# Kernel optimization log

Measured on AMD Instinct MI355X. Metric: run time of the kernel, lower is better.

Reference implementation:

```python
import jax, jax.numpy as jnp
import numpy as np

N, D, O, H, T, S, R, BN = 4096, 256, 256, 256, 512, 8, 4, 2  # nodes, in, out, hidden, text_len, adj_size, relations used, basis_num


def setup_inputs() -> dict:
    key = jax.random.key(0)
    ks = jax.random.split(key, 16)
    sc = 0.05
    return {
        "entity_embeddings": jax.random.normal(ks[0], (N, D), jnp.float32) * sc,
        "text_encodings": jax.random.normal(ks[1], (1, T, 2 * H), jnp.float32) * sc,
        "adj_to_use": jnp.arange(R, dtype=jnp.int32),
        "adj_masks": jax.random.randint(ks[2], (R, N, N), 0, 2, dtype=jnp.int32),
        "text_guids": jax.random.normal(ks[3], (S, 2 * H), jnp.float32) * sc,
        "graph_guids_1": jax.random.normal(ks[4], (S, D), jnp.float32) * sc,
        "graph_guids_2": jax.random.normal(ks[5], (S, D), jnp.float32) * sc,
        "guid_a": jax.random.normal(ks[6], (S,), jnp.float32),
        "basis_V": jax.random.normal(ks[7], (D, BN, O), jnp.float32) * sc,
        "basis_b": jax.random.normal(ks[8], (S, BN), jnp.float32) * sc,
        "W_1": jax.random.normal(ks[9], (2 * H, D), jnp.float32) * sc,
        "W_2": jax.random.normal(ks[10], (2 * H, D), jnp.float32) * sc,
        "ln_gamma": jnp.ones((O,), jnp.float32),
        "ln_beta": jnp.zeros((O,), jnp.float32),
    }


def reference(entity_embeddings, text_encodings, adj_to_use, adj_masks,
              text_guids, graph_guids_1, graph_guids_2, guid_a,
              basis_V, basis_b, W_1, W_2, ln_gamma, ln_beta):
    te = text_encodings[0]                                  # [T, 2H] (batch of 1)
    tg = text_guids[adj_to_use]                             # [R, 2H]
    # text attention: softmax over T, per relation
    att = jax.nn.softmax(te @ tg.T, axis=0)                 # [T, R]
    context = att.T @ te                                    # [R, 2H]
    c1 = context @ W_1                                      # [R, D]
    c2 = context @ W_2
    ga = jax.nn.sigmoid(guid_a[adj_to_use])[:, None]        # [R, 1]
    g1 = ga * graph_guids_1[adj_to_use] + (1.0 - ga) * c1   # [R, D]
    g2 = ga * graph_guids_2[adj_to_use] + (1.0 - ga) * c2
    s1 = entity_embeddings @ g1.T                           # [N, R]
    s2 = entity_embeddings @ g2.T
    # A[r,i,j] = s1[i,r] + s2[j,r], masked softmax over j
    A = s1.T[:, :, None] + s2.T[:, None, :]                 # [R, N, N]
    A = jnp.where(adj_masks == 1, A, jnp.float32(-1e10))
    A = jax.nn.softmax(A, axis=-1)
    fused = jnp.einsum('rij,jd->rid', A, entity_embeddings) # [R, N, D]
    # torch.cat over relations on last dim -> column index r*D + d
    fused_cat = jnp.transpose(fused, (1, 0, 2)).reshape(N, R * D)
    # torch.matmul([R,BN],[D,BN,O]) -> [D,R,O], then .view(R*D, O) (row index d*R + r)
    bb = basis_b[adj_to_use]                                # [R, BN]
    W = jnp.einsum('rb,dbo->dro', bb, basis_V).reshape(D * R, O)
    out = fused_cat @ W                                     # [N, O]
    mu = jnp.mean(out, axis=-1, keepdims=True)
    var = jnp.var(out, axis=-1, keepdims=True)
    out = (out - mu) / jnp.sqrt(var + 1e-5) * ln_gamma + ln_beta
    return jax.nn.relu(out)
```

## Files before the change

### kernel.cpp

```cpp
#include <hip/hip_runtime.h>
#include <hip/hip_bf16.h>


typedef unsigned short u16;
typedef short bf16x8 __attribute__((ext_vector_type(8)));
typedef float f32x4 __attribute__((ext_vector_type(4)));
typedef int   v4i   __attribute__((ext_vector_type(4)));
typedef unsigned int v2u __attribute__((ext_vector_type(2)));

#define G2_OFF    0
#define E2_OFF    4096
#define WRT_OFF   69632
#define FPT_OFF   593920
#define FUSED_OFF 9506816
#define CAN_OFF   26284032
#define ATT_OFF   29443584
#define CTX_OFF   29451776

#define C_ENT 0
#define C_TE  1048576
#define C_TG  1310720
#define C_GG2 1314816
#define C_GA  1316864
#define C_BV  1316872
#define C_BB  1447944
#define C_W2  1447960
#define C_GAM 1579032
#define C_BET 1579288

__device__ __forceinline__ float b2f(u16 u) {
    union { unsigned int i; float f; } v; v.i = ((unsigned int)u) << 16; return v.f;
}
__device__ __forceinline__ u16 f2b(float f) {
    union { float f; unsigned int i; } v; v.f = f;
    return (u16)((v.i + 0x7FFFu + ((v.i >> 16) & 1u)) >> 16);
}
__device__ __forceinline__ void bsync() {
    __builtin_amdgcn_s_waitcnt(0xC07F);
    __builtin_amdgcn_s_barrier();
}

__global__ __launch_bounds__(256) void k_cvt(
    const void* s0, const void* s1, const void* s2, const void* s3,
    const void* s4, const void* s5, const void* s6, const void* s7,
    const void* s8, const void* s9, const unsigned* __restrict__ graw,
    u16* __restrict__ dst)
{
    bool isbf = (graw[0] == 0x3F803F80u);
    const void* srcs[10] = {s0, s1, s2, s3, s4, s5, s6, s7, s8, s9};
    const int ns[10]     = {1048576, 262144, 4096, 2048, 8, 131072, 16, 131072, 256, 256};
    const int offs[10]   = {C_ENT, C_TE, C_TG, C_GG2, C_GA, C_BV, C_BB, C_W2, C_GAM, C_BET};
    const int bstart[11] = {0, 512, 640, 642, 643, 644, 708, 709, 773, 774, 775};
    int b = blockIdx.x, a = 0;
    while (b >= bstart[a + 1]) ++a;
    int rel = b - bstart[a];
    int n = ns[a];
    u16* d = dst + offs[a];
    int base = rel * 2048 + threadIdx.x;
    if (isbf) {
        const u16* s = (const u16*)srcs[a];
        for (int k = 0; k < 8; ++k) { int i = base + k * 256; if (i < n) d[i] = s[i]; }
    } else {
        const float* s = (const float*)srcs[a];
        for (int k = 0; k < 8; ++k) { int i = base + k * 256; if (i < n) d[i] = f2b(s[i]); }
    }
}

__global__ __launch_bounds__(512) void k_pre(const u16* __restrict__ te,
                                             const int* __restrict__ adj,
                                             const u16* __restrict__ tguids,
                                             float* __restrict__ att_ws) {
    __shared__ float s_tg[4 * 512];
    __shared__ float s_att[512 * 4];
    __shared__ float s_red[512 * 4];
    int tid = threadIdx.x;
    int a[4] = {adj[0], adj[1], adj[2], adj[3]};
    for (int k = 0; k < 4; ++k) {
        int idx = tid + k * 512; int r = idx >> 9, h = idx & 511;
        s_tg[r * 512 + h] = b2f(tguids[a[r] * 512 + h]);
    }
    __syncthreads();
    {
        float s[4] = {0.f, 0.f, 0.f, 0.f};
        const u16* row = te + tid * 512;
        for (int h8 = 0; h8 < 512; h8 += 8) {
            v4i pk = *(const v4i*)(row + h8);
            const u16* pu = (const u16*)&pk;
            #pragma unroll
            for (int j = 0; j < 8; ++j) {
                float tv = b2f(pu[j]);
                s[0] += tv * s_tg[h8 + j];        s[1] += tv * s_tg[512 + h8 + j];
                s[2] += tv * s_tg[1024 + h8 + j]; s[3] += tv * s_tg[1536 + h8 + j];
            }
        }
        for (int r = 0; r < 4; ++r) { s_att[tid * 4 + r] = s[r]; s_red[tid * 4 + r] = s[r]; }
    }
    __syncthreads();
    for (int st = 256; st > 0; st >>= 1) {
        if (tid < st) for (int r = 0; r < 4; ++r)
            s_red[tid * 4 + r] = fmaxf(s_red[tid * 4 + r], s_red[(tid + st) * 4 + r]);
        __syncthreads();
    }
    float mx[4]; for (int r = 0; r < 4; ++r) mx[r] = s_red[r];
    __syncthreads();
    for (int r = 0; r < 4; ++r) {
        float e = __expf(s_att[tid * 4 + r] - mx[r]);
        s_att[tid * 4 + r] = e; s_red[tid * 4 + r] = e;
    }
    __syncthreads();
    for (int st = 256; st > 0; st >>= 1) {
        if (tid < st) for (int r = 0; r < 4; ++r)
            s_red[tid * 4 + r] += s_red[(tid + st) * 4 + r];
        __syncthreads();
    }
    float dn[4]; for (int r = 0; r < 4; ++r) dn[r] = s_red[r];
    for (int r = 0; r < 4; ++r) att_ws[tid * 4 + r] = s_att[tid * 4 + r] / dn[r];
}

__global__ __launch_bounds__(256) void k_ctx(const u16* __restrict__ te,
                                             const float* __restrict__ att,
                                             float* __restrict__ ctx) {
    __shared__ float s_att[2048];
    int tid = threadIdx.x, b = blockIdx.x;
    for (int k = 0; k < 8; ++k) s_att[tid + k * 256] = att[tid + k * 256];
    __syncthreads();
    int r = tid >> 6, h = b * 64 + (tid & 63);
    float acc = 0.f;
    #pragma unroll 4
    for (int t = 0; t < 512; ++t) acc += s_att[t * 4 + r] * b2f(te[t * 512 + h]);
    ctx[r * 512 + h] = acc;
}

__global__ __launch_bounds__(256) void k_g2(const float* __restrict__ ctx,
                                            const int* __restrict__ adj,
                                            const u16* __restrict__ gg2,
                                            const u16* __restrict__ guida,
                                            const u16* __restrict__ W2,
                                            float* __restrict__ g2ws) {
    __shared__ float s_c[512];
    int r = blockIdx.x, d = threadIdx.x;
    s_c[d] = ctx[r * 512 + d]; s_c[d + 256] = ctx[r * 512 + 256 + d];
    __syncthreads();
    float acc = 0.f;
    #pragma unroll 4
    for (int h = 0; h < 512; ++h) acc += s_c[h] * b2f(W2[h * 256 + d]);
    int a = adj[r];
    float gav = 1.f / (1.f + expf(-b2f(guida[a])));
    g2ws[r * 256 + d] = gav * b2f(gg2[a * 256 + d]) + (1.f - gav) * acc;
}

__global__ __launch_bounds__(256) void k_s2_wrt(const u16* __restrict__ entity,
                                                const int* __restrict__ adj,
                                                const u16* __restrict__ basisV,
                                                const u16* __restrict__ basisb,
                                                const float* __restrict__ g2ws,
                                                float* __restrict__ e2ws,
                                                u16* __restrict__ wrt) {
    int b = blockIdx.x, tid = threadIdx.x;
    if (b < 64) {
        int j = b * 64 + (tid >> 2), r = tid & 3;
        const u16* erow = entity + j * 256;
        const float* g2r = g2ws + r * 256;
        float acc = 0.f;
        for (int d = 0; d < 256; ++d) acc += b2f(erow[d]) * g2r[d];
        e2ws[r * 4096 + j] = expf(acc);
    } else {
        int b2 = b - 64; int r = b2 >> 6;
        int c = (b2 & 63) * 4 + (tid >> 6);
        int dq = tid & 63;
        int dbase = dq * 4;
        int a[4] = {adj[0], adj[1], adj[2], adj[3]};
        for (int dd = 0; dd < 4; ++dd) {
            float w = 0.f;
            for (int bi = 0; bi < 2; ++bi)
                w += b2f(basisb[a[dd] * 2 + bi]) * b2f(basisV[((64 * r + dq) * 2 + bi) * 256 + c]);
            wrt[(r * 256 + c) * 256 + dbase + dd] = f2b(w);
        }
    }
}

__global__ __launch_bounds__(256) void k_fplus(const u16* __restrict__ entity,
                                               const u16* __restrict__ wrt,
                                               const float* __restrict__ e2ws,
                                               u16* __restrict__ fpt) {
    int b = blockIdx.x, tid = threadIdx.x;
    if (b < 256) {
        int r = b & 3, ct = (b >> 2) & 3, jt = b >> 4;
        int c0 = ct * 64, j0 = jt * 256;
        __shared__ __align__(16) u16 lw[64 * 264];
        const u16* wr = wrt + (r * 256 + c0) * 256;
        for (int k = 0; k < 8; ++k) {
            int ci = tid + k * 256; int row = ci >> 5, off = (ci & 31) * 8;
            *(v4i*)(&lw[row * 264 + off]) = *(const v4i*)(wr + row * 256 + off);
        }
        __syncthreads();
        int wave = tid >> 6, ln = tid & 15, q = (tid & 63) >> 4;
        f32x4 acc[4][4] = {};
        for (int ks = 0; ks < 8; ++ks) {
            bf16x8 afr[4], bfr[4];
            for (int mt = 0; mt < 4; ++mt)
                afr[mt] = *(const bf16x8*)(&lw[(mt * 16 + ln) * 264 + ks * 32 + q * 8]);
            for (int nt = 0; nt < 4; ++nt) {
                int j = j0 + (wave * 4 + nt) * 16 + ln;
                bfr[nt] = *(const bf16x8*)(entity + j * 256 + ks * 32 + q * 8);
            }
            for (int mt = 0; mt < 4; ++mt)
                for (int nt = 0; nt < 4; ++nt)
                    acc[mt][nt] = __builtin_amdgcn_mfma_f32_16x16x32_bf16(afr[mt], bfr[nt], acc[mt][nt], 0, 0, 0);
        }
        for (int nt = 0; nt < 4; ++nt) {
            int j = j0 + (wave * 4 + nt) * 16 + ln;
            float e2j = e2ws[r * 4096 + j];
            int kt = j >> 5, kk = j & 31;
            u16* dst = fpt + (((size_t)(r * 128 + kt)) * 272 << 5);
            for (int mt = 0; mt < 4; ++mt)
                for (int reg = 0; reg < 4; ++reg) {
                    int c = c0 + mt * 16 + q * 4 + reg;
                    dst[(c << 5) + kk] = f2b(acc[mt][nt][reg] * e2j);
                }
        }
    } else {
        int b2 = b - 256; int r = b2 >> 1, half = b2 & 1;
        const float* e2r = e2ws + r * 4096;
        for (int it = 0; it < 128; ++it) {
            int l = it * 256 + tid;
            int kk = l & 31;
            int c  = 256 + ((l >> 5) & 15);
            int kt = half * 64 + (l >> 9);
            fpt[(((size_t)(r * 128 + kt) * 272 + c) << 5) + kk] =
                (c == 256) ? f2b(e2r[kt * 32 + kk]) : (u16)0;
        }
    }
}

__global__ __launch_bounds__(512) void k_big(const int* __restrict__ masks,
                                             const u16* __restrict__ fpt,
                                             float* __restrict__ fused) {
    __shared__ __align__(16) u16 lm2[2][64 * 32];
    __shared__ __align__(16) u16 lf2[2][272 * 32];
    __shared__ float lden[64];
    int b = blockIdx.x, tid = threadIdx.x;
    int xcd = b & 7; int r = xcd & 3;
    int it = (b >> 3) + ((xcd >> 2) << 5);
    long i0 = (long)it * 64;
    const int* mbase = masks + ((long)r << 24) + i0 * 4096;
    const u16* fbase = fpt + (size_t)r * 128 * 272 * 32;
    int mrow = tid >> 3, mch = tid & 7;
    int wave = tid >> 6, lane = tid & 63, ln = lane & 15, q = lane >> 4;
    int mg = wave >> 2, ng = wave & 3;

    f32x4 acc[2][4] = {};
    f32x4 accD0 = {}, accD1 = {};

    v4i pmA, p0A, p1A, p2A, pmB, p0B, p1B, p2B;
    auto load_set = [&](int kt, v4i& pm_, v4i& p0, v4i& p1, v4i& p2) {
        pm_ = __builtin_nontemporal_load((const v4i*)(mbase + mrow * 4096 + kt * 32 + mch * 4));
        const u16* su = fbase + (size_t)kt * 8704;
        p0 = *(const v4i*)(su + tid * 8);
        p1 = *(const v4i*)(su + 4096 + tid * 8);
        if (tid < 64) p2 = *(const v4i*)(su + 8192 + tid * 8);
    };
    auto write_set = [&](int buf, const v4i& pm_, const v4i& p0, const v4i& p1, const v4i& p2) {
        unsigned m0 = (unsigned)pm_.x * 0x3F80u, m1 = (unsigned)pm_.y * 0x3F80u;
        unsigned m2 = (unsigned)pm_.z * 0x3F80u, m3 = (unsigned)pm_.w * 0x3F80u;
        v2u w; w.x = m0 | (m1 << 16); w.y = m2 | (m3 << 16);
        *(v2u*)(&lm2[buf][mrow * 32 + mch * 4]) = w;
        *(v4i*)(&lf2[buf][tid * 8]) = p0;
        *(v4i*)(&lf2[buf][4096 + tid * 8]) = p1;
        if (tid < 64) *(v4i*)(&lf2[buf][8192 + tid * 8]) = p2;
    };
    auto mfma_step = [&](int buf) {
        const u16* lm = lm2[buf];
        const u16* lf = lf2[buf];
        bf16x8 a0 = *(const bf16x8*)(lm + (mg * 32 + ln) * 32 + q * 8);
        bf16x8 a1 = *(const bf16x8*)(lm + (mg * 32 + 16 + ln) * 32 + q * 8);
        #pragma unroll
        for (int nt = 0; nt < 4; ++nt) {
            bf16x8 bf = *(const bf16x8*)(lf + ((ng * 4 + nt) * 16 + ln) * 32 + q * 8);
            acc[0][nt] = __builtin_amdgcn_mfma_f32_16x16x32_bf16(a0, bf, acc[0][nt], 0, 0, 0);
            acc[1][nt] = __builtin_amdgcn_mfma_f32_16x16x32_bf16(a1, bf, acc[1][nt], 0, 0, 0);
        }
        if (ng == 3) {
            bf16x8 bf = *(const bf16x8*)(lf + (256 + ln) * 32 + q * 8);
            accD0 = __builtin_amdgcn_mfma_f32_16x16x32_bf16(a0, bf, accD0, 0, 0, 0);
            accD1 = __builtin_amdgcn_mfma_f32_16x16x32_bf16(a1, bf, accD1, 0, 0, 0);
        }
    };

    load_set(0, pmA, p0A, p1A, p2A);
    load_set(1, pmB, p0B, p1B, p2B);
    write_set(0, pmA, p0A, p1A, p2A);
    load_set(2, pmA, p0A, p1A, p2A);
    bsync();

    #pragma unroll 1
    for (int kt = 0; kt < 128; kt += 2) {
        write_set(1, pmB, p0B, p1B, p2B);
        if (kt + 3 < 128) load_set(kt + 3, pmB, p0B, p1B, p2B);
        mfma_step(0);
        bsync();
        if (kt + 2 < 128) write_set(0, pmA, p0A, p1A, p2A);
        if (kt + 4 < 128) load_set(kt + 4, pmA, p0A, p1A, p2A);
        mfma_step(1);
        bsync();
    }

    if (ng == 3 && ln == 0) {
        #pragma unroll
        for (int reg = 0; reg < 4; ++reg) {
            lden[mg * 32 + q * 4 + reg]      = accD0[reg];
            lden[mg * 32 + 16 + q * 4 + reg] = accD1[reg];
        }
    }
    bsync();
    float* fb = fused + ((long)r * 4096 + i0) * 256;
    #pragma unroll
    for (int mt = 0; mt < 2; ++mt) {
        float rd[4];
        #pragma unroll
        for (int reg = 0; reg < 4; ++reg) rd[reg] = 1.0f / lden[mg * 32 + mt * 16 + q * 4 + reg];
        #pragma unroll
        for (int nt = 0; nt < 4; ++nt) {
            int c = (ng * 4 + nt) * 16 + ln;
            #pragma unroll
            for (int reg = 0; reg < 4; ++reg) {
                int row = mg * 32 + mt * 16 + q * 4 + reg;
                __builtin_nontemporal_store(acc[mt][nt][reg] * rd[reg], fb + row * 256 + c);
            }
        }
    }
}

__global__ __launch_bounds__(256) void k_ln(const float* __restrict__ fused,
                                            const u16* __restrict__ gamma,
                                            const u16* __restrict__ beta,
                                            const unsigned* __restrict__ graw,
                                            void* __restrict__ outraw) {
    __shared__ float wsum[4], wsum2[4];
    int i = blockIdx.x, o = threadIdx.x, w = o >> 6, l = o & 63;
    float x = 0.f;
    for (int r = 0; r < 4; ++r)
        x += __builtin_nontemporal_load(fused + ((long)(r << 12) + i) * 256 + o);
    float s = x, s2 = x * x;
    #pragma unroll
    for (int d = 1; d < 64; d <<= 1) { s += __shfl_xor(s, d); s2 += __shfl_xor(s2, d); }
    if (l == 0) { wsum[w] = s; wsum2[w] = s2; }
    __syncthreads();
    float tot  = wsum[0] + wsum[1] + wsum[2] + wsum[3];
    float tot2 = wsum2[0] + wsum2[1] + wsum2[2] + wsum2[3];
    float mu = tot * (1.f / 256.f);
    float var = tot2 * (1.f / 256.f) - mu * mu;
    float y = (x - mu) * rsqrtf(var + 1e-5f) * b2f(gamma[o]) + b2f(beta[o]);
    float res = fmaxf(y, 0.f);
    bool isbf = (graw[0] == 0x3F803F80u);
    if (isbf) ((u16*)outraw)[i * 256 + o] = f2b(res);
    else      ((float*)outraw)[i * 256 + o] = res;
}

extern "C" void kernel_launch(void* const* d_in, const int* in_sizes, int n_in,
                              void* d_out, int out_size, void* d_ws, size_t ws_size,
                              hipStream_t stream) {
    const int* adj   = (const int*)d_in[2];
    const int* masks = (const int*)d_in[3];
    const unsigned* graw = (const unsigned*)d_in[12];
    char* ws = (char*)d_ws;
    float* g2ws = (float*)(ws + G2_OFF);
    float* e2ws = (float*)(ws + E2_OFF);
    u16*   wrt  = (u16*)(ws + WRT_OFF);
    u16*   fpt  = (u16*)(ws + FPT_OFF);
    float* fus  = (float*)(ws + FUSED_OFF);
    u16*   can  = (u16*)(ws + CAN_OFF);
    float* attw = (float*)(ws + ATT_OFF);
    float* ctxw = (float*)(ws + CTX_OFF);

    k_cvt<<<775, 256, 0, stream>>>(d_in[0], d_in[1], d_in[4], d_in[6], d_in[7],
                                   d_in[8], d_in[9], d_in[11], d_in[12], d_in[13],
                                   graw, can);
    const u16* entity = can + C_ENT;
    const u16* te     = can + C_TE;
    const u16* tguids = can + C_TG;
    const u16* gg2    = can + C_GG2;
    const u16* guida  = can + C_GA;
    const u16* basisV = can + C_BV;
    const u16* basisb = can + C_BB;
    const u16* W2     = can + C_W2;
    const u16* gamma  = can + C_GAM;
    const u16* beta   = can + C_BET;

    k_pre<<<1, 512, 0, stream>>>(te, adj, tguids, attw);
    k_ctx<<<8, 256, 0, stream>>>(te, attw, ctxw);
    k_g2<<<4, 256, 0, stream>>>(ctxw, adj, gg2, guida, W2, g2ws);
    k_s2_wrt<<<320, 256, 0, stream>>>(entity, adj, basisV, basisb, g2ws, e2ws, wrt);
    k_fplus<<<264, 256, 0, stream>>>(entity, wrt, e2ws, fpt);
    k_big<<<256, 512, 0, stream>>>(masks, fpt, fus);
    k_ln<<<4096, 256, 0, stream>>>(fus, gamma, beta, graw, d_out);
}
```

Baseline: 560.5 us.

## Split k_big K-loop in two halves and read B operand directly from global

The main masked-softmax-aggregation kernel now splits the 4096-long reduction into two halves across twice as many blocks (512 instead of 256). Each half writes unnormalized numerators and denominators to workspace, and the layernorm kernel combines them and divides. The B-operand tile is no longer staged through LDS; waves load it straight from global or L2 into registers, which shrinks shared memory so more blocks fit per CU. This trades doubled partial-output traffic and unbuffered global B loads for more parallelism on the 256-CU device.

```diff
diff --git a/kernel.cpp b/kernel.cpp
--- a/kernel.cpp
+++ b/kernel.cpp
@@ -12,10 +12,11 @@
 #define E2_OFF    4096
 #define WRT_OFF   69632
 #define FPT_OFF   593920
-#define FUSED_OFF 9506816
-#define CAN_OFF   26284032
-#define ATT_OFF   29443584
-#define CTX_OFF   29451776
+#define NUM_OFF   9506816
+#define DEN_OFF   43061248
+#define CAN_OFF   43192320
+#define ATT_OFF   46351424
+#define CTX_OFF   46359616
 
 #define C_ENT 0
 #define C_TE  1048576
@@ -233,18 +234,20 @@
     }
 }
 
-__global__ __launch_bounds__(512) void k_big(const int* __restrict__ masks,
-                                             const u16* __restrict__ fpt,
-                                             float* __restrict__ fused) {
+__global__ __launch_bounds__(512, 4) void k_big(const int* __restrict__ masks,
+                                                const u16* __restrict__ fpt,
+                                                float* __restrict__ num,
+                                                float* __restrict__ den) {
     __shared__ __align__(16) u16 lm2[2][64 * 32];
-    __shared__ __align__(16) u16 lf2[2][272 * 32];
-    __shared__ float lden[64];
     int b = blockIdx.x, tid = threadIdx.x;
     int xcd = b & 7; int r = xcd & 3;
-    int it = (b >> 3) + ((xcd >> 2) << 5);
+    int z = b >> 3;
+    int half = z & 1;
+    int it = (z >> 1) + ((xcd >> 2) << 5);
     long i0 = (long)it * 64;
-    const int* mbase = masks + ((long)r << 24) + i0 * 4096;
-    const u16* fbase = fpt + (size_t)r * 128 * 272 * 32;
+    int k0 = half * 64;
+    const int* mbase = masks + ((long)r << 24) + i0 * 4096 + k0 * 32;
+    const u16* fbase = fpt + (size_t)r * 128 * 8704 + (size_t)k0 * 8704;
     int mrow = tid >> 3, mch = tid & 7;
     int wave = tid >> 6, lane = tid & 63, ln = lane & 15, q = lane >> 4;
     int mg = wave >> 2, ng = wave & 3;
@@ -252,86 +255,79 @@
     f32x4 acc[2][4] = {};
     f32x4 accD0 = {}, accD1 = {};
 
-    v4i pmA, p0A, p1A, p2A, pmB, p0B, p1B, p2B;
-    auto load_set = [&](int kt, v4i& pm_, v4i& p0, v4i& p1, v4i& p2) {
-        pm_ = __builtin_nontemporal_load((const v4i*)(mbase + mrow * 4096 + kt * 32 + mch * 4));
-        const u16* su = fbase + (size_t)kt * 8704;
-        p0 = *(const v4i*)(su + tid * 8);
-        p1 = *(const v4i*)(su + 4096 + tid * 8);
-        if (tid < 64) p2 = *(const v4i*)(su + 8192 + tid * 8);
+    v4i sA, sB;
+    auto loadS = [&](int kt, v4i& s) {
+        s = __builtin_nontemporal_load((const v4i*)(mbase + mrow * 4096 + kt * 32 + mch * 4));
     };
-    auto write_set = [&](int buf, const v4i& pm_, const v4i& p0, const v4i& p1, const v4i& p2) {
-        unsigned m0 = (unsigned)pm_.x * 0x3F80u, m1 = (unsigned)pm_.y * 0x3F80u;
-        unsigned m2 = (unsigned)pm_.z * 0x3F80u, m3 = (unsigned)pm_.w * 0x3F80u;
+    auto writeLM = [&](int buf, const v4i& s) {
+        unsigned m0 = (unsigned)s.x * 0x3F80u, m1 = (unsigned)s.y * 0x3F80u;
+        unsigned m2 = (unsigned)s.z * 0x3F80u, m3 = (unsigned)s.w * 0x3F80u;
         v2u w; w.x = m0 | (m1 << 16); w.y = m2 | (m3 << 16);
         *(v2u*)(&lm2[buf][mrow * 32 + mch * 4]) = w;
-        *(v4i*)(&lf2[buf][tid * 8]) = p0;
-        *(v4i*)(&lf2[buf][4096 + tid * 8]) = p1;
-        if (tid < 64) *(v4i*)(&lf2[buf][8192 + tid * 8]) = p2;
     };
-    auto mfma_step = [&](int buf) {
-        const u16* lm = lm2[buf];
-        const u16* lf = lf2[buf];
-        bf16x8 a0 = *(const bf16x8*)(lm + (mg * 32 + ln) * 32 + q * 8);
-        bf16x8 a1 = *(const bf16x8*)(lm + (mg * 32 + 16 + ln) * 32 + q * 8);
-        #pragma unroll
-        for (int nt = 0; nt < 4; ++nt) {
-            bf16x8 bf = *(const bf16x8*)(lf + ((ng * 4 + nt) * 16 + ln) * 32 + q * 8);
-            acc[0][nt] = __builtin_amdgcn_mfma_f32_16x16x32_bf16(a0, bf, acc[0][nt], 0, 0, 0);
-            acc[1][nt] = __builtin_amdgcn_mfma_f32_16x16x32_bf16(a1, bf, acc[1][nt], 0, 0, 0);
-        }
+    auto compute = [&](int buf, int kt) {
+        const u16* su = fbase + (size_t)kt * 8704;
+        bf16x8 b0 = *(const bf16x8*)(su + ((ng * 4 + 0) * 16 + ln) * 32 + q * 8);
+        bf16x8 b1 = *(const bf16x8*)(su + ((ng * 4 + 1) * 16 + ln) * 32 + q * 8);
+        bf16x8 b2 = *(const bf16x8*)(su + ((ng * 4 + 2) * 16 + ln) * 32 + q * 8);
+        bf16x8 b3 = *(const bf16x8*)(su + ((ng * 4 + 3) * 16 + ln) * 32 + q * 8);
+        bf16x8 a0 = *(const bf16x8*)(&lm2[buf][(mg * 32 + ln) * 32 + q * 8]);
+        bf16x8 a1 = *(const bf16x8*)(&lm2[buf][(mg * 32 + 16 + ln) * 32 + q * 8]);
+        acc[0][0] = __builtin_amdgcn_mfma_f32_16x16x32_bf16(a0, b0, acc[0][0], 0, 0, 0);
+        acc[1][0] = __builtin_amdgcn_mfma_f32_16x16x32_bf16(a1, b0, acc[1][0], 0, 0, 0);
+        acc[0][1] = __builtin_amdgcn_mfma_f32_16x16x32_bf16(a0, b1, acc[0][1], 0, 0, 0);
+        acc[1][1] = __builtin_amdgcn_mfma_f32_16x16x32_bf16(a1, b1, acc[1][1], 0, 0, 0);
+        acc[0][2] = __builtin_amdgcn_mfma_f32_16x16x32_bf16(a0, b2, acc[0][2], 0, 0, 0);
+        acc[1][2] = __builtin_amdgcn_mfma_f32_16x16x32_bf16(a1, b2, acc[1][2], 0, 0, 0);
+        acc[0][3] = __builtin_amdgcn_mfma_f32_16x16x32_bf16(a0, b3, acc[0][3], 0, 0, 0);
+        acc[1][3] = __builtin_amdgcn_mfma_f32_16x16x32_bf16(a1, b3, acc[1][3], 0, 0, 0);
         if (ng == 3) {
-            bf16x8 bf = *(const bf16x8*)(lf + (256 + ln) * 32 + q * 8);
-            accD0 = __builtin_amdgcn_mfma_f32_16x16x32_bf16(a0, bf, accD0, 0, 0, 0);
-            accD1 = __builtin_amdgcn_mfma_f32_16x16x32_bf16(a1, bf, accD1, 0, 0, 0);
+            bf16x8 bd = *(const bf16x8*)(su + (256 + ln) * 32 + q * 8);
+            accD0 = __builtin_amdgcn_mfma_f32_16x16x32_bf16(a0, bd, accD0, 0, 0, 0);
+            accD1 = __builtin_amdgcn_mfma_f32_16x16x32_bf16(a1, bd, accD1, 0, 0, 0);
         }
     };
 
-    load_set(0, pmA, p0A, p1A, p2A);
-    load_set(1, pmB, p0B, p1B, p2B);
-    write_set(0, pmA, p0A, p1A, p2A);
-    load_set(2, pmA, p0A, p1A, p2A);
+    loadS(0, sA); loadS(1, sB);
+    writeLM(0, sA);
+    loadS(2, sA);
     bsync();
-
     #pragma unroll 1
-    for (int kt = 0; kt < 128; kt += 2) {
-        write_set(1, pmB, p0B, p1B, p2B);
-        if (kt + 3 < 128) load_set(kt + 3, pmB, p0B, p1B, p2B);
-        mfma_step(0);
+    for (int kt = 0; kt < 64; kt += 2) {
+        writeLM(1, sB);
+        if (kt + 3 < 64) loadS(kt + 3, sB);
+        compute(0, kt);
         bsync();
-        if (kt + 2 < 128) write_set(0, pmA, p0A, p1A, p2A);
-        if (kt + 4 < 128) load_set(kt + 4, pmA, p0A, p1A, p2A);
-        mfma_step(1);
+        if (kt + 2 < 64) writeLM(0, sA);
+        if (kt + 4 < 64) loadS(kt + 4, sA);
+        compute(1, kt + 1);
         bsync();
     }
 
-    if (ng == 3 && ln == 0) {
-        #pragma unroll
-        for (int reg = 0; reg < 4; ++reg) {
-            lden[mg * 32 + q * 4 + reg]      = accD0[reg];
-            lden[mg * 32 + 16 + q * 4 + reg] = accD1[reg];
-        }
-    }
-    bsync();
-    float* fb = fused + ((long)r * 4096 + i0) * 256;
+    float* nb = num + (((size_t)(half * 4 + r) * 4096) + i0) * 256;
     #pragma unroll
-    for (int mt = 0; mt < 2; ++mt) {
-        float rd[4];
-        #pragma unroll
-        for (int reg = 0; reg < 4; ++reg) rd[reg] = 1.0f / lden[mg * 32 + mt * 16 + q * 4 + reg];
+    for (int mt = 0; mt < 2; ++mt)
         #pragma unroll
         for (int nt = 0; nt < 4; ++nt) {
             int c = (ng * 4 + nt) * 16 + ln;
             #pragma unroll
             for (int reg = 0; reg < 4; ++reg) {
                 int row = mg * 32 + mt * 16 + q * 4 + reg;
-                __builtin_nontemporal_store(acc[mt][nt][reg] * rd[reg], fb + row * 256 + c);
+                __builtin_nontemporal_store(acc[mt][nt][reg], nb + row * 256 + c);
             }
         }
-    }
-}
-
-__global__ __launch_bounds__(256) void k_ln(const float* __restrict__ fused,
+    if (ng == 3 && ln == 0) {
+        float* db = den + ((size_t)(half * 4 + r) * 4096) + i0;
+        #pragma unroll
+        for (int reg = 0; reg < 4; ++reg) {
+            db[mg * 32 + q * 4 + reg]      = accD0[reg];
+            db[mg * 32 + 16 + q * 4 + reg] = accD1[reg];
+        }
+    }
+}
+
+__global__ __launch_bounds__(256) void k_ln(const float* __restrict__ num,
+                                            const float* __restrict__ den,
                                             const u16* __restrict__ gamma,
                                             const u16* __restrict__ beta,
                                             const unsigned* __restrict__ graw,
@@ -339,8 +335,13 @@
     __shared__ float wsum[4], wsum2[4];
     int i = blockIdx.x, o = threadIdx.x, w = o >> 6, l = o & 63;
     float x = 0.f;
-    for (int r = 0; r < 4; ++r)
-        x += __builtin_nontemporal_load(fused + ((long)(r << 12) + i) * 256 + o);
+    #pragma unroll
+    for (int r = 0; r < 4; ++r) {
+        float dsum = den[(size_t)r * 4096 + i] + den[(size_t)(4 + r) * 4096 + i];
+        float n = __builtin_nontemporal_load(num + ((size_t)r * 4096 + i) * 256 + o)
+                + __builtin_nontemporal_load(num + ((size_t)(4 + r) * 4096 + i) * 256 + o);
+        x += n / dsum;
+    }
     float s = x, s2 = x * x;
     #pragma unroll
     for (int d = 1; d < 64; d <<= 1) { s += __shfl_xor(s, d); s2 += __shfl_xor(s2, d); }
@@ -368,7 +369,8 @@
     float* e2ws = (float*)(ws + E2_OFF);
     u16*   wrt  = (u16*)(ws + WRT_OFF);
     u16*   fpt  = (u16*)(ws + FPT_OFF);
-    float* fus  = (float*)(ws + FUSED_OFF);
+    float* numw = (float*)(ws + NUM_OFF);
+    float* denw = (float*)(ws + DEN_OFF);
     u16*   can  = (u16*)(ws + CAN_OFF);
     float* attw = (float*)(ws + ATT_OFF);
     float* ctxw = (float*)(ws + CTX_OFF);
@@ -392,6 +394,6 @@
     k_g2<<<4, 256, 0, stream>>>(ctxw, adj, gg2, guida, W2, g2ws);
     k_s2_wrt<<<320, 256, 0, stream>>>(entity, adj, basisV, basisb, g2ws, e2ws, wrt);
     k_fplus<<<264, 256, 0, stream>>>(entity, wrt, e2ws, fpt);
-    k_big<<<256, 512, 0, stream>>>(masks, fpt, fus);
-    k_ln<<<4096, 256, 0, stream>>>(fus, gamma, beta, graw, d_out);
-}
+    k_big<<<512, 512, 0, stream>>>(masks, fpt, numw, denw);
+    k_ln<<<4096, 256, 0, stream>>>(numw, denw, gamma, beta, graw, d_out);
+}
```

After: 586.8 us. 4.7% more time.

## Drop LDS staging in k_big; load MFMA operands directly from global

Applied to the files above, without the earlier changes.

The main masked-aggregation kernel no longer stages the mask and feature tiles through double-buffered shared memory with barriers. Each wave now loads its own mask rows and B fragments straight from global memory into registers, prefetching one k-step ahead, and converts the int mask to bf16 in registers. Blocks shrink to 256 threads covering 32 rows, with twice as many blocks, removing per-step barriers and LDS traffic. In exchange, the feature tile is re-read from global or L2 by every block and wave without sharing, which risks more memory traffic. Smaller tweaks vectorize the e2 dot-product loads and unroll the LayerNorm relation loop.

```diff
diff --git a/kernel.cpp b/kernel.cpp
--- a/kernel.cpp
+++ b/kernel.cpp
@@ -6,7 +6,6 @@
 typedef short bf16x8 __attribute__((ext_vector_type(8)));
 typedef float f32x4 __attribute__((ext_vector_type(4)));
 typedef int   v4i   __attribute__((ext_vector_type(4)));
-typedef unsigned int v2u __attribute__((ext_vector_type(2)));
 
 #define G2_OFF    0
 #define E2_OFF    4096
@@ -35,9 +34,13 @@
     union { float f; unsigned int i; } v; v.f = f;
     return (u16)((v.i + 0x7FFFu + ((v.i >> 16) & 1u)) >> 16);
 }
-__device__ __forceinline__ void bsync() {
-    __builtin_amdgcn_s_waitcnt(0xC07F);
-    __builtin_amdgcn_s_barrier();
+__device__ __forceinline__ bf16x8 cvt8(v4i lo, v4i hi) {
+    v4i p;
+    p.x = (lo.x | (lo.y << 16)) * 0x3F80;
+    p.y = (lo.z | (lo.w << 16)) * 0x3F80;
+    p.z = (hi.x | (hi.y << 16)) * 0x3F80;
+    p.w = (hi.z | (hi.w << 16)) * 0x3F80;
+    union { v4i i; bf16x8 h; } u; u.i = p; return u.h;
 }
 
 __global__ __launch_bounds__(256) void k_cvt(
@@ -162,7 +165,12 @@
         const u16* erow = entity + j * 256;
         const float* g2r = g2ws + r * 256;
         float acc = 0.f;
-        for (int d = 0; d < 256; ++d) acc += b2f(erow[d]) * g2r[d];
+        for (int d8 = 0; d8 < 256; d8 += 8) {
+            v4i pk = *(const v4i*)(erow + d8);
+            const u16* pu = (const u16*)&pk;
+            #pragma unroll
+            for (int jj = 0; jj < 8; ++jj) acc += b2f(pu[jj]) * g2r[d8 + jj];
+        }
         e2ws[r * 4096 + j] = expf(acc);
     } else {
         int b2 = b - 64; int r = b2 >> 6;
@@ -233,98 +241,89 @@
     }
 }
 
-__global__ __launch_bounds__(512) void k_big(const int* __restrict__ masks,
-                                             const u16* __restrict__ fpt,
-                                             float* __restrict__ fused) {
-    __shared__ __align__(16) u16 lm2[2][64 * 32];
-    __shared__ __align__(16) u16 lf2[2][272 * 32];
-    __shared__ float lden[64];
+__global__ __launch_bounds__(256, 3) void k_big(const int* __restrict__ masks,
+                                                const u16* __restrict__ fpt,
+                                                float* __restrict__ fused) {
+    __shared__ float lden[32];
     int b = blockIdx.x, tid = threadIdx.x;
     int xcd = b & 7; int r = xcd & 3;
-    int it = (b >> 3) + ((xcd >> 2) << 5);
-    long i0 = (long)it * 64;
+    int it = (b >> 3) + ((xcd >> 2) << 6);
+    long i0 = (long)it * 32;
     const int* mbase = masks + ((long)r << 24) + i0 * 4096;
-    const u16* fbase = fpt + (size_t)r * 128 * 272 * 32;
-    int mrow = tid >> 3, mch = tid & 7;
+    const u16* fbase = fpt + (size_t)r * 128 * 8704;
     int wave = tid >> 6, lane = tid & 63, ln = lane & 15, q = lane >> 4;
-    int mg = wave >> 2, ng = wave & 3;
+    int ng = wave;
+
+    const int* a0p = mbase + ln * 4096 + q * 8;
+    const int* a1p = a0p + (16 << 12);
+    const u16* bq = fbase + (size_t)(((ng * 4) * 16 + ln) * 32 + q * 8);
 
     f32x4 acc[2][4] = {};
     f32x4 accD0 = {}, accD1 = {};
 
-    v4i pmA, p0A, p1A, p2A, pmB, p0B, p1B, p2B;
-    auto load_set = [&](int kt, v4i& pm_, v4i& p0, v4i& p1, v4i& p2) {
-        pm_ = __builtin_nontemporal_load((const v4i*)(mbase + mrow * 4096 + kt * 32 + mch * 4));
-        const u16* su = fbase + (size_t)kt * 8704;
-        p0 = *(const v4i*)(su + tid * 8);
-        p1 = *(const v4i*)(su + 4096 + tid * 8);
-        if (tid < 64) p2 = *(const v4i*)(su + 8192 + tid * 8);
+    v4i A0l, A0h, A1l, A1h, nA0l, nA0h, nA1l, nA1h;
+    bf16x8 B0, B1, B2, B3, BD, nB0, nB1, nB2, nB3, nBD;
+    auto loadA = [&](int kt, v4i& x0l, v4i& x0h, v4i& x1l, v4i& x1h) {
+        const int* p0 = a0p + kt * 32;
+        const int* p1 = a1p + kt * 32;
+        x0l = *(const v4i*)p0; x0h = *(const v4i*)(p0 + 4);
+        x1l = *(const v4i*)p1; x1h = *(const v4i*)(p1 + 4);
     };
-    auto write_set = [&](int buf, const v4i& pm_, const v4i& p0, const v4i& p1, const v4i& p2) {
-        unsigned m0 = (unsigned)pm_.x * 0x3F80u, m1 = (unsigned)pm_.y * 0x3F80u;
-        unsigned m2 = (unsigned)pm_.z * 0x3F80u, m3 = (unsigned)pm_.w * 0x3F80u;
-        v2u w; w.x = m0 | (m1 << 16); w.y = m2 | (m3 << 16);
-        *(v2u*)(&lm2[buf][mrow * 32 + mch * 4]) = w;
-        *(v4i*)(&lf2[buf][tid * 8]) = p0;
-        *(v4i*)(&lf2[buf][4096 + tid * 8]) = p1;
-        if (tid < 64) *(v4i*)(&lf2[buf][8192 + tid * 8]) = p2;
+    auto loadB = [&](int kt, bf16x8& y0, bf16x8& y1, bf16x8& y2, bf16x8& y3, bf16x8& yd) {
+        const u16* su = bq + (size_t)kt * 8704;
+        y0 = *(const bf16x8*)(su);
+        y1 = *(const bf16x8*)(su + 16 * 32);
+        y2 = *(const bf16x8*)(su + 32 * 32);
+        y3 = *(const bf16x8*)(su + 48 * 32);
+        if (ng == 3) yd = *(const bf16x8*)(fbase + (size_t)kt * 8704 + (256 + ln) * 32 + q * 8);
     };
-    auto mfma_step = [&](int buf) {
-        const u16* lm = lm2[buf];
-        const u16* lf = lf2[buf];
-        bf16x8 a0 = *(const bf16x8*)(lm + (mg * 32 + ln) * 32 + q * 8);
-        bf16x8 a1 = *(const bf16x8*)(lm + (mg * 32 + 16 + ln) * 32 + q * 8);
-        #pragma unroll
-        for (int nt = 0; nt < 4; ++nt) {
-            bf16x8 bf = *(const bf16x8*)(lf + ((ng * 4 + nt) * 16 + ln) * 32 + q * 8);
-            acc[0][nt] = __builtin_amdgcn_mfma_f32_16x16x32_bf16(a0, bf, acc[0][nt], 0, 0, 0);
-            acc[1][nt] = __builtin_amdgcn_mfma_f32_16x16x32_bf16(a1, bf, acc[1][nt], 0, 0, 0);
-        }
+
+    loadA(0, A0l, A0h, A1l, A1h);
+    loadB(0, B0, B1, B2, B3, BD);
+    #pragma unroll 2
+    for (int kt = 0; kt < 128; ++kt) {
+        if (kt + 1 < 128) {
+            loadA(kt + 1, nA0l, nA0h, nA1l, nA1h);
+            loadB(kt + 1, nB0, nB1, nB2, nB3, nBD);
+        }
+        bf16x8 a0 = cvt8(A0l, A0h), a1 = cvt8(A1l, A1h);
+        acc[0][0] = __builtin_amdgcn_mfma_f32_16x16x32_bf16(a0, B0, acc[0][0], 0, 0, 0);
+        acc[1][0] = __builtin_amdgcn_mfma_f32_16x16x32_bf16(a1, B0, acc[1][0], 0, 0, 0);
+        acc[0][1] = __builtin_amdgcn_mfma_f32_16x16x32_bf16(a0, B1, acc[0][1], 0, 0, 0);
+        acc[1][1] = __builtin_amdgcn_mfma_f32_16x16x32_bf16(a1, B1, acc[1][1], 0, 0, 0);
+        acc[0][2] = __builtin_amdgcn_mfma_f32_16x16x32_bf16(a0, B2, acc[0][2], 0, 0, 0);
+        acc[1][2] = __builtin_amdgcn_mfma_f32_16x16x32_bf16(a1, B2, acc[1][2], 0, 0, 0);
+        acc[0][3] = __builtin_amdgcn_mfma_f32_16x16x32_bf16(a0, B3, acc[0][3], 0, 0, 0);
+        acc[1][3] = __builtin_amdgcn_mfma_f32_16x16x32_bf16(a1, B3, acc[1][3], 0, 0, 0);
         if (ng == 3) {
-            bf16x8 bf = *(const bf16x8*)(lf + (256 + ln) * 32 + q * 8);
-            accD0 = __builtin_amdgcn_mfma_f32_16x16x32_bf16(a0, bf, accD0, 0, 0, 0);
-            accD1 = __builtin_amdgcn_mfma_f32_16x16x32_bf16(a1, bf, accD1, 0, 0, 0);
-        }
-    };
-
-    load_set(0, pmA, p0A, p1A, p2A);
-    load_set(1, pmB, p0B, p1B, p2B);
-    write_set(0, pmA, p0A, p1A, p2A);
-    load_set(2, pmA, p0A, p1A, p2A);
-    bsync();
-
-    #pragma unroll 1
-    for (int kt = 0; kt < 128; kt += 2) {
-        write_set(1, pmB, p0B, p1B, p2B);
-        if (kt + 3 < 128) load_set(kt + 3, pmB, p0B, p1B, p2B);
-        mfma_step(0);
-        bsync();
-        if (kt + 2 < 128) write_set(0, pmA, p0A, p1A, p2A);
-        if (kt + 4 < 128) load_set(kt + 4, pmA, p0A, p1A, p2A);
-        mfma_step(1);
-        bsync();
+            accD0 = __builtin_amdgcn_mfma_f32_16x16x32_bf16(a0, BD, accD0, 0, 0, 0);
+            accD1 = __builtin_amdgcn_mfma_f32_16x16x32_bf16(a1, BD, accD1, 0, 0, 0);
+        }
+        A0l = nA0l; A0h = nA0h; A1l = nA1l; A1h = nA1h;
+        B0 = nB0; B1 = nB1; B2 = nB2; B3 = nB3;
+        if (ng == 3) BD = nBD;
     }
 
     if (ng == 3 && ln == 0) {
         #pragma unroll
         for (int reg = 0; reg < 4; ++reg) {
-            lden[mg * 32 + q * 4 + reg]      = accD0[reg];
-            lden[mg * 32 + 16 + q * 4 + reg] = accD1[reg];
-        }
-    }
-    bsync();
+            lden[q * 4 + reg]      = accD0[reg];
+            lden[16 + q * 4 + reg] = accD1[reg];
+        }
+    }
+    __syncthreads();
     float* fb = fused + ((long)r * 4096 + i0) * 256;
     #pragma unroll
     for (int mt = 0; mt < 2; ++mt) {
         float rd[4];
         #pragma unroll
-        for (int reg = 0; reg < 4; ++reg) rd[reg] = 1.0f / lden[mg * 32 + mt * 16 + q * 4 + reg];
+        for (int reg = 0; reg < 4; ++reg) rd[reg] = 1.0f / lden[mt * 16 + q * 4 + reg];
         #pragma unroll
         for (int nt = 0; nt < 4; ++nt) {
             int c = (ng * 4 + nt) * 16 + ln;
             #pragma unroll
             for (int reg = 0; reg < 4; ++reg) {
-                int row = mg * 32 + mt * 16 + q * 4 + reg;
+                int row = mt * 16 + q * 4 + reg;
                 __builtin_nontemporal_store(acc[mt][nt][reg] * rd[reg], fb + row * 256 + c);
             }
         }
@@ -339,6 +338,7 @@
     __shared__ float wsum[4], wsum2[4];
     int i = blockIdx.x, o = threadIdx.x, w = o >> 6, l = o & 63;
     float x = 0.f;
+    #pragma unroll
     for (int r = 0; r < 4; ++r)
         x += __builtin_nontemporal_load(fused + ((long)(r << 12) + i) * 256 + o);
     float s = x, s2 = x * x;
@@ -392,6 +392,6 @@
     k_g2<<<4, 256, 0, stream>>>(ctxw, adj, gg2, guida, W2, g2ws);
     k_s2_wrt<<<320, 256, 0, stream>>>(entity, adj, basisV, basisb, g2ws, e2ws, wrt);
     k_fplus<<<264, 256, 0, stream>>>(entity, wrt, e2ws, fpt);
-    k_big<<<256, 512, 0, stream>>>(masks, fpt, fus);
+    k_big<<<512, 256, 0, stream>>>(masks, fpt, fus);
     k_ln<<<4096, 256, 0, stream>>>(fus, gamma, beta, graw, d_out);
 }
```

Result: slower. 666.8 us (+19.0%).
